# Kernel tuning notes

Hardware: AMD Instinct MI355X
Metric: run time of the kernel (lower is better)

## Reference

```python
import jax, jax.numpy as jnp
import numpy as np

B, M, N, R, FD = 128, 64, 64, 8, 128
BN_EPS = 1e-5
GS_EPS = 1e-8


def conv2d(x, w, b):
    # x: [B,C,H,W], w: [O,C,3,3] or [O,C,1,1]
    y = jax.lax.conv_general_dilated(x, w, (1, 1), 'SAME',
                                     dimension_numbers=('NCHW', 'OIHW', 'NCHW'))
    return y + b[None, :, None, None]


def complex_conv(x, wr, br, wi, bi):
    cr = conv2d(x, wr, br)
    ci = conv2d(x, wi, bi)
    return jnp.concatenate([cr - ci, cr + ci], axis=1)


def batchnorm(x, g, b):
    # training-mode BN over (B,H,W)
    mean = x.mean(axis=(0, 2, 3), keepdims=True)
    var = ((x - mean) ** 2).mean(axis=(0, 2, 3), keepdims=True)
    return g[None, :, None, None] * (x - mean) * jax.lax.rsqrt(var + BN_EPS) + b[None, :, None, None]


def gram_schmidt(mat):
    # mat: [B, M, R, 2]; sequential over R (hard data dependency), vectorized over batch
    Rr = mat.shape[2]
    basis = []  # list of (vr, vi), each [B, M]
    for j in range(Rr):
        vr, vi = mat[:, :, j, 0], mat[:, :, j, 1]
        for br_, bi_ in basis:
            dot_real = jnp.sum(vr * br_ + vi * bi_, axis=1, keepdims=True)
            denom = jnp.sum(br_ * br_ + bi_ * bi_, axis=1, keepdims=True) + GS_EPS
            coef = dot_real / denom  # only real part used (as in torch code)
            vr = vr - coef * br_
            vi = vi - coef * bi_
        nrm = jnp.sqrt(jnp.sum(vr * vr + vi * vi, axis=1, keepdims=True) + GS_EPS)
        basis.append((vr / nrm, vi / nrm))
    return jnp.stack([jnp.stack(p, axis=-1) for p in basis], axis=2)  # [B,M,R,2]


def setup_inputs() -> dict:
    key = jax.random.key(0)
    ks = jax.random.split(key, 32)
    def p(i, shape, fan_in):
        return jax.random.normal(ks[i], shape, jnp.float32) / np.sqrt(fan_in)
    inp = {
        'x':   jax.random.normal(ks[0], (B, M, N, 2), jnp.float32),
        'w1r': p(1, (32, 2, 3, 3), 2 * 9),   'b1r': jnp.zeros((32,), jnp.float32),
        'w1i': p(2, (32, 2, 3, 3), 2 * 9),   'b1i': jnp.zeros((32,), jnp.float32),
        'g1':  jnp.ones((64,), jnp.float32), 'be1': jnp.zeros((64,), jnp.float32),
        'w2r': p(3, (64, 64, 3, 3), 64 * 9), 'b2r': jnp.zeros((64,), jnp.float32),
        'w2i': p(4, (64, 64, 3, 3), 64 * 9), 'b2i': jnp.zeros((64,), jnp.float32),
        'g2':  jnp.ones((128,), jnp.float32), 'be2': jnp.zeros((128,), jnp.float32),
        'w3r': p(5, (FD, 128, 3, 3), 128 * 9), 'b3r': jnp.zeros((FD,), jnp.float32),
        'w3i': p(6, (FD, 128, 3, 3), 128 * 9), 'b3i': jnp.zeros((FD,), jnp.float32),
        'g3':  jnp.ones((2 * FD,), jnp.float32), 'be3': jnp.zeros((2 * FD,), jnp.float32),
        'wu':  p(7, (2 * R, 2 * FD), 2 * FD), 'bu': jnp.zeros((2 * R,), jnp.float32),
        'ws':  p(8, (R, 2 * FD), 2 * FD),     'bs': jnp.zeros((R,), jnp.float32),
        'wv':  p(9, (2 * R, 2 * FD), 2 * FD), 'bv': jnp.zeros((2 * R,), jnp.float32),
    }
    return inp


def forward(x, w1r, b1r, w1i, b1i, g1, be1, w2r, b2r, w2i, b2i, g2, be2,
            w3r, b3r, w3i, b3i, g3, be3, wu, bu, ws, bs, wv, bv):
    h = jnp.transpose(x, (0, 3, 1, 2))  # [B,2,M,N]
    h = jax.nn.relu(batchnorm(complex_conv(h, w1r, b1r, w1i, b1i), g1, be1))
    h = jax.nn.relu(batchnorm(complex_conv(h, w2r, b2r, w2i, b2i), g2, be2))
    h = jax.nn.relu(batchnorm(complex_conv(h, w3r, b3r, w3i, b3i), g3, be3))  # [B,2FD,M,N]
    # u branch: avg over W, 1x1 conv (= channel matmul), relu
    pu = h.mean(axis=3)                                      # [B,2FD,M]
    u = jax.nn.relu(jnp.einsum('bcm,oc->bom', pu, wu) + bu[None, :, None])  # [B,2R,M]
    u = jnp.transpose(u, (0, 2, 1)).reshape(-1, M, R, 2)     # channel c = 2j+part
    u = gram_schmidt(u)
    # s branch: global avg pool + linear + relu
    ps = h.mean(axis=(2, 3))                                 # [B,2FD]
    s = jax.nn.relu(ps @ ws.T + bs)                          # [B,R]
    # v branch: avg over H, 1x1 conv, relu
    pv = h.mean(axis=2)                                      # [B,2FD,N]
    v = jax.nn.relu(jnp.einsum('bcn,oc->bon', pv, wv) + bv[None, :, None])  # [B,2R,N]
    v = jnp.transpose(v, (0, 2, 1)).reshape(-1, N, R, 2)
    v = gram_schmidt(v)
    return (u, s, v)


def reference(x, w1r, b1r, w1i, b1i, g1, be1, w2r, b2r, w2i, b2i, g2, be2,
              w3r, b3r, w3i, b3i, g3, be3, wu, bu, ws, bs, wv, bv):
    return forward(x, w1r, b1r, w1i, b1i, g1, be1, w2r, b2r, w2i, b2i, g2, be2,
                   w3r, b3r, w3i, b3i, g3, be3, wu, bu, ws, bs, wv, bv)
```

## Files before the change

kernel.cpp:

```cpp
#include <hip/hip_runtime.h>

typedef _Float16 f16;
typedef __attribute__((ext_vector_type(8))) short short8;
typedef __attribute__((ext_vector_type(8))) _Float16 half8;
typedef __attribute__((ext_vector_type(4))) float f32x4;

#define DEV __device__ __forceinline__

DEV float h2f(short s) { f16 h; __builtin_memcpy(&h, &s, 2); return (float)h; }
DEV short f2h(float f) { f16 h = (f16)f; short s; __builtin_memcpy(&s, &h, 2); return s; }
DEV half8 s2h8(short8 s) { half8 h; __builtin_memcpy(&h, &s, 16); return h; }

DEV float wave_sum(float v) {
    #pragma unroll
    for (int m = 1; m < 64; m <<= 1) v += __shfl_xor(v, m);
    return v;
}

__global__ __launch_bounds__(256) void prep_w_k(
    const float* __restrict__ wr, const float* __restrict__ wi,
    f16* __restrict__ wf, int CIN, int COUT)
{
    int idx = blockIdx.x * 256 + threadIdx.x;
    int KC = CIN >> 5, NG = (2 * COUT) >> 4;
    int total = 9 * KC * NG * 512;
    if (idx >= total) return;
    int j = idx & 7, lane = (idx >> 3) & 63;
    int t9 = idx >> 9;
    int gg = t9 % NG, s = t9 / NG;
    int tap = s % 9, kc = s / 9;
    int n = gg * 16 + (lane & 15);
    int cin = kc * 32 + (lane >> 4) * 8 + j;
    int o = n < COUT ? n : n - COUT;
    float sgn = n < COUT ? -1.f : 1.f;
    float wv = wr[(o * CIN + cin) * 9 + tap] + sgn * wi[(o * CIN + cin) * 9 + tap];
    wf[idx] = (f16)wv;
}

__global__ __launch_bounds__(256) void conv1_k(
    const float* __restrict__ x,
    const float* __restrict__ w1r, const float* __restrict__ w1i,
    f16* __restrict__ out)
{
    int idx = blockIdx.x * 256 + threadIdx.x;
    int b = idx >> 12, p = idx & 4095;
    int m = p >> 6, n = p & 63;

    float v[2][9];
    #pragma unroll
    for (int dy = 0; dy < 3; ++dy)
        #pragma unroll
        for (int dx = 0; dx < 3; ++dx) {
            int yy = m + dy - 1, xx = n + dx - 1;
            bool ok = (yy >= 0 && yy < 64 && xx >= 0 && xx < 64);
            int base = ((b * 64 + (ok ? yy : 0)) * 64 + (ok ? xx : 0)) * 2;
            v[0][dy*3+dx] = ok ? x[base]     : 0.f;
            v[1][dy*3+dx] = ok ? x[base + 1] : 0.f;
        }

    float o1[64];
    #pragma unroll
    for (int o = 0; o < 32; ++o) {
        float cr = 0.f, ci = 0.f;
        #pragma unroll
        for (int c = 0; c < 2; ++c)
            #pragma unroll
            for (int k = 0; k < 9; ++k) {
                cr = fmaf(v[c][k], w1r[(o*2+c)*9 + k], cr);
                ci = fmaf(v[c][k], w1i[(o*2+c)*9 + k], ci);
            }
        o1[o]      = cr - ci;
        o1[32 + o] = cr + ci;
    }
    f16* ob = out + (size_t)idx * 64;
    #pragma unroll
    for (int grp = 0; grp < 8; ++grp) {
        short8 pk;
        #pragma unroll
        for (int k = 0; k < 8; ++k) pk[k] = f2h(o1[grp*8 + k]);
        *(short8*)(ob + grp * 8) = pk;
    }
}

template<int C8>
__global__ __launch_bounds__(256) void statsv_k(
    const f16* __restrict__ t, float* __restrict__ stats, int iters)
{
    const int C = C8 * 8;
    __shared__ float ls[2 * C];
    const int tid = threadIdx.x;
    const int cg = tid & (C8 - 1), pg = tid / C8;
    const int NG = 256 / C8;
    for (int u = tid; u < 2 * C; u += 256) ls[u] = 0.f;
    __syncthreads();
    float s8[8] = {0,0,0,0,0,0,0,0}, q8[8] = {0,0,0,0,0,0,0,0};
    size_t base = (size_t)blockIdx.x * NG * iters + pg;
    for (int i = 0; i < iters; ++i) {
        size_t pp = base + (size_t)i * NG;
        short8 r = *(const short8*)(t + pp * C + cg * 8);
        #pragma unroll
        for (int k = 0; k < 8; ++k) { float v = h2f(r[k]); s8[k] += v; q8[k] += v * v; }
    }
    #pragma unroll
    for (int k = 0; k < 8; ++k) {
        atomicAdd(&ls[cg*8 + k], s8[k]);
        atomicAdd(&ls[C + cg*8 + k], q8[k]);
    }
    __syncthreads();
    for (int u = tid; u < C; u += 256) {
        atomicAdd(&stats[u], ls[u]);
        atomicAdd(&stats[C + u], ls[C + u]);
    }
}

__global__ void bnparam_k(const float* __restrict__ stats,
                          const float* __restrict__ g, const float* __restrict__ be,
                          float* __restrict__ sc, int C)
{
    int c = threadIdx.x;
    if (c >= C) return;
    const float invN = 1.f / (128.f * 4096.f);
    float mean  = stats[c] * invN;
    float var   = stats[C + c] * invN - mean * mean;
    float scale = g[c] * rsqrtf(var + 1e-5f);
    sc[c]     = scale;
    sc[C + c] = be[c] - mean * scale;
}

template<int CIN, bool CHUNK>
__global__ __launch_bounds__(256, 2) void conv_mfma_k(
    const f16* __restrict__ in, const f16* __restrict__ wf,
    const float* __restrict__ scin, f16* __restrict__ outp,
    float* __restrict__ stats, int n0, int NG, int statsC, int ostride)
{
    constexpr int KQ = CIN / 32;
    constexpr int NSTEP = KQ * 9;
    __shared__ char actl[10*66*32*2];
    __shared__ float lsts[4][64], lstq[4][64];
    const int flat = blockIdx.x;
    const int swzb = (flat & 7) * 128 + (flat >> 3);
    const int b = swzb >> 3, y0 = (swzb & 7) * 8;
    const int n0e = n0 + blockIdx.y * 64;
    const int tid = threadIdx.x, l = tid & 63, w = tid >> 6;
    const int li = l & 15, g = l >> 4;

    f32x4 acc[8][4];
    #pragma unroll
    for (int mf = 0; mf < 8; ++mf)
        #pragma unroll
        for (int nf = 0; nf < 4; ++nf)
            acc[mf][nf] = f32x4{0.f, 0.f, 0.f, 0.f};

    int swz[3];
    #pragma unroll
    for (int dx = 0; dx < 3; ++dx) swz[dx] = ((li + dx) & 7) << 4;

    const f16* wblk = wf + ((size_t)(n0e >> 4) << 9) + (l << 3);

    for (int st = 0; st < NSTEP; ++st) {
        const int kq = st / 9, tap = st - kq * 9;
        if (tap == 0) {
            half8 scl8, shf8;
            {
                int cb = kq*32 + (tid & 3) * 8;
                #pragma unroll
                for (int k = 0; k < 8; ++k) {
                    scl8[k] = (f16)scin[cb + k];
                    shf8[k] = (f16)scin[CIN + cb + k];
                }
            }
            __syncthreads();
            #pragma unroll
            for (int i = 0; i < 11; ++i) {
                int u = tid + i * 256;
                if (u < 10*66*4) {
                    int r = u / 264, rem = u - r * 264;
                    int sx = rem >> 2, cg = rem & 3;
                    int srow = y0 - 1 + r, gx = sx - 1;
                    short8 pk = {0,0,0,0,0,0,0,0};
                    if (srow >= 0 && srow < 64 && gx >= 0 && gx < 64) {
                        short8 raw = *(const short8*)(in +
                            ((size_t)(b*4096 + srow*64 + gx)) * CIN + kq*32 + cg*8);
                        half8 rv = s2h8(raw) * scl8 + shf8;
                        short8 sr; __builtin_memcpy(&sr, &rv, 16);
                        pk = sr & ~(sr >> 15);
                    }
                    int off = ((r*66 + sx)*32 + cg*8)*2 ^ ((sx & 7) << 4);
                    *(short8*)(actl + off) = pk;
                }
            }
            __syncthreads();
        }
        short8 breg[4];
        {
            int s = kq * 9 + tap;
            const f16* p = wblk + ((size_t)(s * NG) << 9);
            #pragma unroll
            for (int nf = 0; nf < 4; ++nf) breg[nf] = *(const short8*)(p + (nf << 9));
        }
        int dy = (tap * 11) >> 5, dx = tap - dy * 3;
        #pragma unroll
        for (int mf = 0; mf < 8; ++mf) {
            int r = 2*w + (mf >> 2) + dy;
            int sx = (mf & 3)*16 + li + dx;
            half8 a = s2h8(*(const short8*)(actl + ((((r*66 + sx)*32) + g*8)*2 ^ swz[dx])));
            #pragma unroll
            for (int nf = 0; nf < 4; ++nf)
                acc[mf][nf] = __builtin_amdgcn_mfma_f32_16x16x32_f16(a, s2h8(breg[nf]), acc[mf][nf], 0, 0, 0);
        }
    }

    #pragma unroll
    for (int nf = 0; nf < 4; ++nf) {
        float s = 0.f, q = 0.f;
        #pragma unroll
        for (int mf = 0; mf < 8; ++mf)
            #pragma unroll
            for (int reg = 0; reg < 4; ++reg) {
                float v = acc[mf][nf][reg];
                s += v; q += v * v;
            }
        s += __shfl_xor(s, 16); s += __shfl_xor(s, 32);
        q += __shfl_xor(q, 16); q += __shfl_xor(q, 32);
        if (l < 16) { lsts[w][nf*16 + l] = s; lstq[w][nf*16 + l] = q; }
    }
    __syncthreads();
    if (tid < 64) {
        const int sb = CHUNK ? 0 : n0e;
        float s = lsts[0][tid] + lsts[1][tid] + lsts[2][tid] + lsts[3][tid];
        float q = lstq[0][tid] + lstq[1][tid] + lstq[2][tid] + lstq[3][tid];
        atomicAdd(&stats[sb + tid], s);
        atomicAdd(&stats[statsC + sb + tid], q);
    }

    const int obase = CHUNK ? 0 : n0e;
    #pragma unroll
    for (int mf = 0; mf < 8; ++mf) {
        size_t rowbase = (size_t)b * 4096 + (size_t)(y0 + 2*w + (mf >> 2)) * 64;
        #pragma unroll
        for (int nf = 0; nf < 4; ++nf) {
            int n = obase + nf*16 + li;
            #pragma unroll
            for (int reg = 0; reg < 4; ++reg) {
                int xx = (mf & 3)*16 + g*4 + reg;
                outp[(rowbase + xx) * ostride + n] = (f16)acc[mf][nf][reg];
            }
        }
    }
}

__global__ __launch_bounds__(256) void pool_k(
    const f16* __restrict__ t3c, const float* __restrict__ sc3c,
    float* __restrict__ pu, float* __restrict__ pv, int ncb)
{
    const int b = blockIdx.x, yh = blockIdx.y;
    const int t = threadIdx.x, cg = t & 7, xp = t >> 3;
    const int w = t >> 6, lane = t & 63;
    __shared__ float rq[4][16][64];
    float scl[8], shf[8];
    #pragma unroll
    for (int k = 0; k < 8; ++k) { scl[k] = sc3c[cg*8 + k]; shf[k] = sc3c[64 + cg*8 + k]; }
    float colacc[2][8];
    #pragma unroll
    for (int xi = 0; xi < 2; ++xi)
        #pragma unroll
        for (int k = 0; k < 8; ++k) colacc[xi][k] = 0.f;

    for (int yb = 0; yb < 2; ++yb) {
        for (int yy = 0; yy < 16; ++yy) {
            int y = yh*32 + yb*16 + yy;
            float rc[8];
            #pragma unroll
            for (int xi = 0; xi < 2; ++xi) {
                int xx = xp*2 + xi;
                short8 raw = *(const short8*)(t3c +
                    ((size_t)(b*4096 + y*64 + xx)) * 64 + cg*8);
                #pragma unroll
                for (int k = 0; k < 8; ++k) {
                    float v = fmaxf(fmaf(h2f(raw[k]), scl[k], shf[k]), 0.f);
                    colacc[xi][k] += v;
                    rc[k] = xi ? (rc[k] + v) : v;
                }
            }
            #pragma unroll
            for (int k = 0; k < 8; ++k) {
                rc[k] += __shfl_xor(rc[k], 8);
                rc[k] += __shfl_xor(rc[k], 16);
                rc[k] += __shfl_xor(rc[k], 32);
            }
            if (lane < 8) {
                #pragma unroll
                for (int k = 0; k < 8; ++k) rq[w][yy][lane*8 + k] = rc[k];
            }
        }
        __syncthreads();
        for (int u = t; u < 1024; u += 256) {
            int yy = u >> 6, c = u & 63;
            float v = rq[0][yy][c] + rq[1][yy][c] + rq[2][yy][c] + rq[3][yy][c];
            pu[((size_t)b*256 + ncb + c)*64 + (yh*32 + yb*16 + yy)] = v * (1.f/64.f);
        }
        __syncthreads();
    }
    #pragma unroll
    for (int xi = 0; xi < 2; ++xi)
        #pragma unroll
        for (int k = 0; k < 8; ++k)
            atomicAdd(&pv[((size_t)b*256 + ncb + cg*8 + k)*64 + xp*2 + xi],
                      colacc[xi][k] * (1.f/64.f));
}

__global__ __launch_bounds__(256) void headuv_k(
    const float* __restrict__ pool, const float* __restrict__ w,
    const float* __restrict__ bias, float* __restrict__ out)
{
    int b = blockIdx.x;
    int m = threadIdx.x & 63;
    int ob4 = threadIdx.x >> 6;
    float acc[4] = { bias[ob4], bias[ob4+4], bias[ob4+8], bias[ob4+12] };
    const float* pb = pool + (size_t)b * 256 * 64 + m;
    for (int c = 0; c < 256; ++c) {
        float v = pb[c * 64];
        #pragma unroll
        for (int i = 0; i < 4; ++i)
            acc[i] = fmaf(v, w[(ob4 + i*4) * 256 + c], acc[i]);
    }
    float* op = out + (size_t)b * 16 * 64 + m;
    #pragma unroll
    for (int i = 0; i < 4; ++i)
        op[(ob4 + i*4) * 64] = fmaxf(acc[i], 0.f);
}

__global__ __launch_bounds__(64) void heads_s_k(
    const float* __restrict__ pu, const float* __restrict__ wS,
    const float* __restrict__ bS, float* __restrict__ out)
{
    int b = blockIdx.x, lane = threadIdx.x;
    __shared__ float ls[256];
    for (int i = 0; i < 4; ++i) {
        const float* p = pu + ((size_t)b*256 + lane*4 + i) * 64;
        float s = 0.f;
        for (int m = 0; m < 64; ++m) s += p[m];
        ls[lane*4 + i] = s * (1.f/64.f);
    }
    __syncthreads();
    float acc[8] = {0,0,0,0,0,0,0,0};
    for (int c = lane; c < 256; c += 64) {
        float v = ls[c];
        #pragma unroll
        for (int o = 0; o < 8; ++o) acc[o] = fmaf(v, wS[o*256 + c], acc[o]);
    }
    #pragma unroll
    for (int o = 0; o < 8; ++o) acc[o] = wave_sum(acc[o]);
    if (lane == 0) {
        #pragma unroll
        for (int o = 0; o < 8; ++o)
            out[b*8 + o] = fmaxf(acc[o] + bS[o], 0.f);
    }
}

__global__ __launch_bounds__(64) void gs_k(
    const float* __restrict__ pre, float* __restrict__ out)
{
    int b = blockIdx.x, lane = threadIdx.x;
    const float* pb = pre + (size_t)b * 16 * 64 + lane;
    float vr[8], vi[8], den[8];
    #pragma unroll
    for (int j = 0; j < 8; ++j) { vr[j] = pb[(2*j)*64]; vi[j] = pb[(2*j+1)*64]; }

    #pragma unroll
    for (int j = 0; j < 8; ++j) {
        #pragma unroll
        for (int k = 0; k < j; ++k) {
            float d = wave_sum(vr[j]*vr[k] + vi[j]*vi[k]);
            float coef = d / den[k];
            vr[j] = fmaf(-coef, vr[k], vr[j]);
            vi[j] = fmaf(-coef, vi[k], vi[j]);
        }
        float n2 = wave_sum(vr[j]*vr[j] + vi[j]*vi[j]);
        float inv = 1.f / sqrtf(n2 + 1e-8f);
        vr[j] *= inv; vi[j] *= inv;
        float nn = wave_sum(vr[j]*vr[j] + vi[j]*vi[j]);
        den[j] = nn + 1e-8f;
    }
    float* ob = out + (size_t)b * 64 * 16 + lane * 16;
    #pragma unroll
    for (int j = 0; j < 8; ++j) { ob[j*2] = vr[j]; ob[j*2+1] = vi[j]; }
}

extern "C" void kernel_launch(void* const* d_in, const int* in_sizes, int n_in,
                              void* d_out, int out_size, void* d_ws, size_t ws_size,
                              hipStream_t stream)
{
    const float* x   = (const float*)d_in[0];
    const float* w1r = (const float*)d_in[1];
    const float* w1i = (const float*)d_in[3];
    const float* g1  = (const float*)d_in[5];
    const float* be1 = (const float*)d_in[6];
    const float* w2r = (const float*)d_in[7];
    const float* w2i = (const float*)d_in[9];
    const float* g2  = (const float*)d_in[11];
    const float* be2 = (const float*)d_in[12];
    const float* w3r = (const float*)d_in[13];
    const float* w3i = (const float*)d_in[15];
    const float* g3  = (const float*)d_in[17];
    const float* be3 = (const float*)d_in[18];
    const float* wu  = (const float*)d_in[19];
    const float* bu  = (const float*)d_in[20];
    const float* wS  = (const float*)d_in[21];
    const float* bS  = (const float*)d_in[22];
    const float* wv  = (const float*)d_in[23];
    const float* bv  = (const float*)d_in[24];
    float* out = (float*)d_out;

    char* ws = (char*)d_ws;
    f16*   t2     = (f16*)  (ws + 0);
    f16*   t1     = (f16*)  (ws + 134217728);
    f16*   t3c    = (f16*)  (ws + 134217728);
    float* upre   = (float*)(ws + 134217728);
    float* vpre   = (float*)(ws + 134742016);
    float* pu     = (float*)(ws + 201326592);
    float* pv     = (float*)(ws + 209715200);
    f16*   wfrag2 = (f16*)  (ws + 218103808);
    f16*   wfrag3 = (f16*)  (ws + 218103808);
    float* stats  = (float*)(ws + 219283456);
    float* scsh   = (float*)(ws + 219287040);
    float* stats1 = stats,  *stats2 = stats + 128;
    float* sc1    = scsh,   *sc2    = scsh  + 128, *sc3c = scsh + 384;

    hipMemsetAsync(stats, 0, 3584, stream);
    hipMemsetAsync(pv, 0, (size_t)128*256*64*4, stream);

    prep_w_k<<<288, 256, 0, stream>>>(w2r, w2i, wfrag2, 64, 64);

    conv1_k<<<2048, 256, 0, stream>>>(x, w1r, w1i, t1);
    statsv_k<8><<<1024, 256, 0, stream>>>(t1, stats1, 16);
    bnparam_k<<<1, 64, 0, stream>>>(stats1, g1, be1, sc1, 64);

    conv_mfma_k<64, false><<<dim3(1024, 2), 256, 0, stream>>>(
        t1, wfrag2, sc1, t2, stats2,
        0, 8, 128, 128);
    bnparam_k<<<1, 128, 0, stream>>>(stats2, g2, be2, sc2, 128);

    prep_w_k<<<1152, 256, 0, stream>>>(w3r, w3i, wfrag3, 128, 128);
    for (int nc = 0; nc < 4; ++nc) {
        conv_mfma_k<128, true><<<dim3(1024, 1), 256, 0, stream>>>(
            t2, wfrag3, sc2, t3c, stats + 384 + nc*128,
            nc*64, 16, 64, 64);
        bnparam_k<<<1, 64, 0, stream>>>(stats + 384 + nc*128, g3 + nc*64, be3 + nc*64, sc3c, 64);
        pool_k<<<dim3(128, 2), 256, 0, stream>>>(t3c, sc3c, pu, pv, nc*64);
    }

    headuv_k<<<128, 256, 0, stream>>>(pu, wu, bu, upre);
    headuv_k<<<128, 256, 0, stream>>>(pv, wv, bv, vpre);
    heads_s_k<<<128, 64, 0, stream>>>(pu, wS, bS, out + 131072);

    gs_k<<<128, 64, 0, stream>>>(upre, out);
    gs_k<<<128, 64, 0, stream>>>(vpre, out + 132096);
}
```

Baseline: 787.6 us.

## Enlarge conv blocks to 512 threads and prefetch weight fragments

```diff
diff --git a/kernel.cpp b/kernel.cpp
--- a/kernel.cpp
+++ b/kernel.cpp
@@ -128,20 +128,25 @@
 }
 
 template<int CIN, bool CHUNK>
-__global__ __launch_bounds__(256, 2) void conv_mfma_k(
+__global__ __launch_bounds__(512, 2) void conv_mfma_k(
     const f16* __restrict__ in, const f16* __restrict__ wf,
     const float* __restrict__ scin, f16* __restrict__ outp,
     float* __restrict__ stats, int n0, int NG, int statsC, int ostride)
 {
     constexpr int KQ = CIN / 32;
     constexpr int NSTEP = KQ * 9;
-    __shared__ char actl[10*66*32*2];
-    __shared__ float lsts[4][64], lstq[4][64];
+    constexpr int NH   = CHUNK ? 1 : 2;
+    constexpr int RW   = 8 / NH;
+    constexpr int ROWS = 2 * RW;
+    constexpr int SROWS = ROWS + 2;
+    constexpr int YT   = 64 / ROWS;
+    __shared__ char actl[SROWS*66*32*2];
+    __shared__ float lsts[8][64], lstq[8][64];
     const int flat = blockIdx.x;
-    const int swzb = (flat & 7) * 128 + (flat >> 3);
-    const int b = swzb >> 3, y0 = (swzb & 7) * 8;
-    const int n0e = n0 + blockIdx.y * 64;
+    const int swzb = (flat & 7) * (128*YT/8) + (flat >> 3);
+    const int b = swzb / YT, y0 = (swzb % YT) * ROWS;
     const int tid = threadIdx.x, l = tid & 63, w = tid >> 6;
+    const int rp = w / NH, nh = w % NH;
     const int li = l & 15, g = l >> 4;
 
     f32x4 acc[8][4];
@@ -155,7 +160,14 @@
     #pragma unroll
     for (int dx = 0; dx < 3; ++dx) swz[dx] = ((li + dx) & 7) << 4;
 
-    const f16* wblk = wf + ((size_t)(n0e >> 4) << 9) + (l << 3);
+    const f16* wblk = wf + ((size_t)((n0 >> 4) + nh*4) << 9) + (l << 3);
+    auto bload = [&](int st, short8* dst) {
+        const f16* p = wblk + ((size_t)(st * NG) << 9);
+        #pragma unroll
+        for (int nf = 0; nf < 4; ++nf) dst[nf] = *(const short8*)(p + (nf << 9));
+    };
+    short8 breg[4], nbreg[4];
+    bload(0, breg);
 
     for (int st = 0; st < NSTEP; ++st) {
         const int kq = st / 9, tap = st - kq * 9;
@@ -171,9 +183,9 @@
             }
             __syncthreads();
             #pragma unroll
-            for (int i = 0; i < 11; ++i) {
-                int u = tid + i * 256;
-                if (u < 10*66*4) {
+            for (int i = 0; i < (SROWS*66*4 + 511)/512; ++i) {
+                int u = tid + i * 512;
+                if (u < SROWS*66*4) {
                     int r = u / 264, rem = u - r * 264;
                     int sx = rem >> 2, cg = rem & 3;
                     int srow = y0 - 1 + r, gx = sx - 1;
@@ -191,23 +203,21 @@
             }
             __syncthreads();
         }
-        short8 breg[4];
-        {
-            int s = kq * 9 + tap;
-            const f16* p = wblk + ((size_t)(s * NG) << 9);
-            #pragma unroll
-            for (int nf = 0; nf < 4; ++nf) breg[nf] = *(const short8*)(p + (nf << 9));
-        }
+        if (st + 1 < NSTEP) bload(st + 1, nbreg);
         int dy = (tap * 11) >> 5, dx = tap - dy * 3;
+        __builtin_amdgcn_s_setprio(1);
         #pragma unroll
         for (int mf = 0; mf < 8; ++mf) {
-            int r = 2*w + (mf >> 2) + dy;
+            int r = 2*rp + (mf >> 2) + dy;
             int sx = (mf & 3)*16 + li + dx;
             half8 a = s2h8(*(const short8*)(actl + ((((r*66 + sx)*32) + g*8)*2 ^ swz[dx])));
             #pragma unroll
             for (int nf = 0; nf < 4; ++nf)
                 acc[mf][nf] = __builtin_amdgcn_mfma_f32_16x16x32_f16(a, s2h8(breg[nf]), acc[mf][nf], 0, 0, 0);
         }
+        __builtin_amdgcn_s_setprio(0);
+        #pragma unroll
+        for (int nf = 0; nf < 4; ++nf) breg[nf] = nbreg[nf];
     }
 
     #pragma unroll
@@ -225,18 +235,22 @@
         if (l < 16) { lsts[w][nf*16 + l] = s; lstq[w][nf*16 + l] = q; }
     }
     __syncthreads();
-    if (tid < 64) {
-        const int sb = CHUNK ? 0 : n0e;
-        float s = lsts[0][tid] + lsts[1][tid] + lsts[2][tid] + lsts[3][tid];
-        float q = lstq[0][tid] + lstq[1][tid] + lstq[2][tid] + lstq[3][tid];
-        atomicAdd(&stats[sb + tid], s);
-        atomicAdd(&stats[statsC + sb + tid], q);
-    }
-
-    const int obase = CHUNK ? 0 : n0e;
+    if (tid < NH*64) {
+        int ch64 = tid & 63, half = tid >> 6;
+        float s = 0.f, q = 0.f;
+        #pragma unroll
+        for (int j = 0; j < RW; ++j) {
+            s += lsts[j*NH + half][ch64];
+            q += lstq[j*NH + half][ch64];
+        }
+        atomicAdd(&stats[tid], s);
+        atomicAdd(&stats[statsC + tid], q);
+    }
+
+    const int obase = nh * 64;
     #pragma unroll
     for (int mf = 0; mf < 8; ++mf) {
-        size_t rowbase = (size_t)b * 4096 + (size_t)(y0 + 2*w + (mf >> 2)) * 64;
+        size_t rowbase = (size_t)b * 4096 + (size_t)(y0 + 2*rp + (mf >> 2)) * 64;
         #pragma unroll
         for (int nf = 0; nf < 4; ++nf) {
             int n = obase + nf*16 + li;
@@ -436,14 +450,14 @@
     statsv_k<8><<<1024, 256, 0, stream>>>(t1, stats1, 16);
     bnparam_k<<<1, 64, 0, stream>>>(stats1, g1, be1, sc1, 64);
 
-    conv_mfma_k<64, false><<<dim3(1024, 2), 256, 0, stream>>>(
+    conv_mfma_k<64, false><<<1024, 512, 0, stream>>>(
         t1, wfrag2, sc1, t2, stats2,
         0, 8, 128, 128);
     bnparam_k<<<1, 128, 0, stream>>>(stats2, g2, be2, sc2, 128);
 
     prep_w_k<<<1152, 256, 0, stream>>>(w3r, w3i, wfrag3, 128, 128);
     for (int nc = 0; nc < 4; ++nc) {
-        conv_mfma_k<128, true><<<dim3(1024, 1), 256, 0, stream>>>(
+        conv_mfma_k<128, true><<<512, 512, 0, stream>>>(
             t2, wfrag3, sc2, t3c, stats + 384 + nc*128,
             nc*64, 16, 64, 64);
         bnparam_k<<<1, 64, 0, stream>>>(stats + 384 + nc*128, g3 + nc*64, be3 + nc*64, sc3c, 64);
```

Measured after the change: 771.3 us. 1.02x faster.
